# Performance work log

Hardware: AMD Instinct MI355X
Metric: run time of the kernel (lower is better)

## Reference

```python
import jax, jax.numpy as jnp
import numpy as np

B, N, F = 32, 64, 128          # batch, num_nodes, n_in_node
K, H, M, NH = 4, 256, 256, 256 # edge_types, msg_hid, msg_out, n_hid
E = N * (N - 1)                # fully-connected directed edges = 4032


def setup_inputs() -> dict:
    key = jax.random.key(0)
    ks = jax.random.split(key, 12)
    inputs = jax.random.normal(ks[0], (B, N, F), dtype=jnp.float32)
    # soft edge-type assignment per edge (rows sum to 1, as in NRI)
    rel_type = jax.nn.softmax(jax.random.normal(ks[1], (B, E, K), dtype=jnp.float32), axis=-1)
    # one-hot receiver/sender matrices for all i != j pairs
    idx = np.array([(i, j) for i in range(N) for j in range(N) if i != j], dtype=np.int64)
    eye = np.eye(N, dtype=np.float32)
    rel_rec = jnp.asarray(eye[idx[:, 0]])   # [E, N]
    rel_send = jnp.asarray(eye[idx[:, 1]])  # [E, N]
    # per-edge-type message MLP weights (stacked over K): y = x @ W + b
    W1 = jax.random.normal(ks[2], (K, 2 * F, H), dtype=jnp.float32) / np.sqrt(2 * F)
    b1 = jnp.zeros((K, H), dtype=jnp.float32)
    W2 = jax.random.normal(ks[3], (K, H, M), dtype=jnp.float32) / np.sqrt(H)
    b2 = jnp.zeros((K, M), dtype=jnp.float32)
    # output MLP
    Wo1 = jax.random.normal(ks[4], (F + M, NH), dtype=jnp.float32) / np.sqrt(F + M)
    bo1 = jnp.zeros((NH,), dtype=jnp.float32)
    Wo2 = jax.random.normal(ks[5], (NH, NH), dtype=jnp.float32) / np.sqrt(NH)
    bo2 = jnp.zeros((NH,), dtype=jnp.float32)
    Wo3 = jax.random.normal(ks[6], (NH, F), dtype=jnp.float32) / np.sqrt(NH)
    bo3 = jnp.zeros((F,), dtype=jnp.float32)
    return {"inputs": inputs, "rel_type": rel_type, "rel_rec": rel_rec, "rel_send": rel_send,
            "W1": W1, "b1": b1, "W2": W2, "b2": b2,
            "Wo1": Wo1, "bo1": bo1, "Wo2": Wo2, "bo2": bo2, "Wo3": Wo3, "bo3": bo3}


def reference(inputs, rel_type, rel_rec, rel_send, W1, b1, W2, b2, Wo1, bo1, Wo2, bo2, Wo3, bo3):
    # gather node states to edges via one-hot matmul (as in the source)
    receivers = jnp.einsum('en,bnf->bef', rel_rec, inputs)   # [B,E,F]
    senders = jnp.einsum('en,bnf->bef', rel_send, inputs)    # [B,E,F]
    pre_msg = jnp.concatenate([receivers, senders], axis=-1)  # [B,E,2F]
    # per-edge-type 2-layer ReLU MLP, batched over the K edge types
    h = jax.nn.relu(jnp.einsum('bef,kfh->bkeh', pre_msg, W1) + b1[:, None, :])  # [B,K,E,H]
    msg = jax.nn.relu(jnp.einsum('bkeh,khm->bkem', h, W2) + b2[:, None, :])     # [B,K,E,M]
    # mask by soft edge type and accumulate over types (dropout p=0 -> identity)
    all_msgs = jnp.einsum('bkem,bek->bem', msg, rel_type)     # [B,E,M]
    # scatter-aggregate messages to receiver nodes via one-hot matmul
    agg_msgs = jnp.einsum('en,bem->bnm', rel_rec, all_msgs)   # [B,N,M]
    aug = jnp.concatenate([inputs, agg_msgs], axis=-1)        # [B,N,F+M]
    p = jax.nn.relu(aug @ Wo1 + bo1)
    p = jax.nn.relu(p @ Wo2 + bo2)
    p = p @ Wo3 + bo3
    return inputs + p
```

## Files before the change

### kernel.cpp

```cpp
#include <hip/hip_runtime.h>


#define B_ 32
#define N_ 64
#define F_ 128
#define K_ 4
#define E_ 4032

#define WS_W2T 0u
#define WS_R   524288u
#define WS_S   4718592u
#define WS_AGG 8912896u

typedef unsigned short u16;
typedef u16    u16x4  __attribute__((ext_vector_type(4)));
typedef u16    u16x8  __attribute__((ext_vector_type(8)));
typedef __bf16 bf16x8 __attribute__((ext_vector_type(8)));
typedef float  f32x4  __attribute__((ext_vector_type(4)));
typedef float  f32x16 __attribute__((ext_vector_type(16)));

__device__ __forceinline__ u16 f2bf(float f) {
    unsigned u; __builtin_memcpy(&u, &f, 4);
    return (u16)((u + 0x7FFFu + ((u >> 16) & 1u)) >> 16);
}
__device__ __forceinline__ float bf2f(u16 u) {
    unsigned v = ((unsigned)u) << 16;
    float f; __builtin_memcpy(&f, &v, 4); return f;
}

#define LBAR() do { \
    asm volatile("s_waitcnt lgkmcnt(0)" ::: "memory"); \
    __builtin_amdgcn_s_barrier(); \
    __builtin_amdgcn_sched_barrier(0); \
} while (0)

__global__ __launch_bounds__(256) void prep_rs_kernel(
    const float* __restrict__ W2, const float* __restrict__ x,
    const float* __restrict__ W1, const float* __restrict__ b1,
    u16* __restrict__ W2t, u16* __restrict__ R, u16* __restrict__ S)
{
    __shared__ u16 ldsA[64 * 136];
    __shared__ u16 ldsW[32 * 136];
    const int tid = threadIdx.x;

    if (blockIdx.x < 1024) {
        unsigned gid = blockIdx.x * 256u + tid;
        unsigned chunk = gid >> 13, r = gid & 8191u;
        unsigned g = r >> 11, n = (r >> 3) & 255u, e = r & 7u;
        unsigned k = chunk >> 3, kc = chunk & 7u, ks2 = g >> 1, lhh = g & 1u;
        unsigned kk = kc * 32u + ks2 * 16u + lhh * 8u + e;
        W2t[gid] = f2bf(W2[(k * 256u + kk) * 256u + n]);
        return;
    }

    const int lane = tid & 63, w = tid >> 6;
    const int quad = lane >> 4, mloc = lane & 15;
    const int bx = blockIdx.x - 1024;
    const int k = bx >> 6, half = (bx >> 5) & 1, b = bx & 31;

    for (int idx = tid; idx < 2048; idx += 256) {
        int row = idx >> 5, c4 = idx & 31;
        f32x4 v = *(const f32x4*)&x[(b * 64 + row) * 128 + c4 * 4];
        u16x4 o;
#pragma unroll
        for (int e = 0; e < 4; ++e) o[e] = f2bf(v[e]);
        *(u16x4*)&ldsA[row * 136 + c4 * 4] = o;
    }
    __syncthreads();

    bf16x8 aF[4];
#pragma unroll
    for (int ks = 0; ks < 4; ++ks)
        aF[ks] = *(const bf16x8*)&ldsA[(w * 16 + mloc) * 136 + quad * 8 + ks * 32];

    u16* dst = half ? S : R;
    for (int c = 0; c < 8; ++c) {
        __syncthreads();
        for (int idx = tid; idx < 4096; idx += 256) {
            int n = idx & 31, f = idx >> 5;
            ldsW[n * 136 + f] = f2bf(W1[(k * 256 + half * 128 + f) * 256 + c * 32 + n]);
        }
        __syncthreads();
#pragma unroll
        for (int nt = 0; nt < 2; ++nt) {
            f32x4 acc = (f32x4){0.f, 0.f, 0.f, 0.f};
            const int boff = (nt * 16 + mloc) * 136 + quad * 8;
#pragma unroll
            for (int ks = 0; ks < 4; ++ks)
                acc = __builtin_amdgcn_mfma_f32_16x16x32_bf16(
                    aF[ks], *(const bf16x8*)&ldsW[boff + ks * 32], acc, 0, 0, 0);
            const int n = c * 32 + nt * 16 + mloc;
            const float bias = half ? 0.f : b1[k * 256 + n];
#pragma unroll
            for (int r = 0; r < 4; ++r) {
                int row = w * 16 + quad * 4 + r;
                if (half) {
                    dst[((size_t)((k * 8 + c) * 2048 + b * 64 + row)) * 32 + nt * 16 + mloc]
                        = f2bf(acc[r] + bias);
                } else {
                    dst[((size_t)(k * 2048 + b * 64 + row)) * 256 + n] = f2bf(acc[r] + bias);
                }
            }
        }
    }
}

__global__ __launch_bounds__(256, 3) void edge12_kernel(
    const u16* __restrict__ R, const u16* __restrict__ S2,
    const float* __restrict__ rel, const u16* __restrict__ W2t,
    const float* __restrict__ b2, u16* __restrict__ aggb)
{
    __shared__ u16   Hs[32][64][8];
    __shared__ float Rf[4][256];
    __shared__ float rtS[4][64];

    const int tid  = threadIdx.x;
    const int lane = tid & 63;
    const int w    = tid >> 6;
    const int l31  = lane & 31;
    const int lh   = lane >> 5;
    const int bid  = ((blockIdx.x & 7) << 8) | (blockIdx.x >> 3);
    const int b    = bid >> 6;
    const int i    = bid & 63;

    {
        const int k = tid >> 6, j = tid & 63;
        float v = 0.f;
        if (j != i) v = rel[((size_t)(b * E_) + i * 63 + (j - (j > i))) * 4 + k];
        rtS[k][j] = v;
    }
    {
        const int k = tid >> 6, e4 = tid & 63;
        u16x4 t4 = *(const u16x4*)&R[((size_t)(k * 2048 + b * 64 + i)) * 256 + e4 * 4];
#pragma unroll
        for (int e = 0; e < 4; ++e) Rf[k][e4 * 4 + e] = bf2f(t4[e]);
    }

    u16x8 sreg[8];
#pragma unroll
    for (int s = 0; s < 8; ++s)
        sreg[s] = *(const u16x8*)&S2[((size_t)(s * 2048 + b * 64 + lane)) * 32 + w * 8];

    __syncthreads();

    const u16* Wb = W2t + lh * 2048 + (w * 64 + l31) * 8;

    float amsg[2] = {0.f, 0.f};

    for (int kT = 0; kT < 4; ++kT) {
        bf16x8 Bb[2][2][2];
#pragma unroll
        for (int ks2 = 0; ks2 < 2; ++ks2) {
            const u16* wp = Wb + (size_t)(kT * 8) * 8192 + ks2 * 4096;
            Bb[0][ks2][0] = *(const bf16x8*)(wp);
            Bb[0][ks2][1] = *(const bf16x8*)(wp + 256);
        }
#pragma unroll
        for (int s = 0; s < 8; ++s) {
            const float* rp = &Rf[kT][s * 32 + w * 8];
            f32x4 r0 = *(const f32x4*)rp, r1 = *(const f32x4*)(rp + 4);
            bf16x8 o;
#pragma unroll
            for (int e = 0; e < 4; ++e) {
                o[e]     = (__bf16)fmaxf(r0[e] + bf2f(sreg[s][e]),     0.f);
                o[4 + e] = (__bf16)fmaxf(r1[e] + bf2f(sreg[s][4 + e]), 0.f);
            }
            *(bf16x8*)&Hs[s * 4 + w][lane][0] = o;
        }
        __syncthreads();

        f32x16 acc[2][2];
#pragma unroll
        for (int mt = 0; mt < 2; ++mt)
#pragma unroll
            for (int nt = 0; nt < 2; ++nt) acc[mt][nt] = (f32x16)(0.f);

#pragma unroll
        for (int kc = 0; kc < 8; ++kc) {
            const int cur = kc & 1, nxt = cur ^ 1;
            if (kc == 0 && kT < 3) {
#pragma unroll
                for (int s = 0; s < 8; ++s)
                    sreg[s] = *(const u16x8*)&S2[((size_t)(((kT + 1) * 8 + s) * 2048 + b * 64 + lane)) * 32 + w * 8];
            }
            if (kc < 7) {
#pragma unroll
                for (int ks2 = 0; ks2 < 2; ++ks2) {
                    const u16* wp = Wb + (size_t)(kT * 8 + kc + 1) * 8192 + ks2 * 4096;
                    Bb[nxt][ks2][0] = *(const bf16x8*)(wp);
                    Bb[nxt][ks2][1] = *(const bf16x8*)(wp + 256);
                }
            }
#pragma unroll
            for (int ks2 = 0; ks2 < 2; ++ks2) {
                const int g = kc * 4 + ks2 * 2 + lh;
                bf16x8 A0 = *(const bf16x8*)&Hs[g][l31][0];
                bf16x8 A1 = *(const bf16x8*)&Hs[g][32 + l31][0];
                acc[0][0] = __builtin_amdgcn_mfma_f32_32x32x16_bf16(A0, Bb[cur][ks2][0], acc[0][0], 0, 0, 0);
                acc[0][1] = __builtin_amdgcn_mfma_f32_32x32x16_bf16(A0, Bb[cur][ks2][1], acc[0][1], 0, 0, 0);
                acc[1][0] = __builtin_amdgcn_mfma_f32_32x32x16_bf16(A1, Bb[cur][ks2][0], acc[1][0], 0, 0, 0);
                acc[1][1] = __builtin_amdgcn_mfma_f32_32x32x16_bf16(A1, Bb[cur][ks2][1], acc[1][1], 0, 0, 0);
            }
        }

#pragma unroll
        for (int nt = 0; nt < 2; ++nt) {
            const float bias = b2[kT * 256 + w * 64 + nt * 32 + l31];
#pragma unroll
            for (int mt = 0; mt < 2; ++mt) {
                float s = 0.f;
#pragma unroll
                for (int rq = 0; rq < 4; ++rq) {
                    f32x4 rt4 = *(const f32x4*)&rtS[kT][mt * 32 + rq * 8 + 4 * lh];
#pragma unroll
                    for (int e = 0; e < 4; ++e) {
                        float v = acc[mt][nt][rq * 4 + e] + bias;
                        v = v > 0.f ? v : 0.f;
                        s += rt4[e] * v;
                    }
                }
                amsg[nt] += s;
            }
        }
        __syncthreads();
    }

#pragma unroll
    for (int nt = 0; nt < 2; ++nt) {
        float s = amsg[nt] + __shfl_xor(amsg[nt], 32);
        if (lh == 0)
            aggb[(size_t)(b * 64 + i) * 256 + w * 64 + nt * 32 + l31] = f2bf(s);
    }
}

__global__ __launch_bounds__(512) void outmlp4_kernel(
    const float* __restrict__ x, const u16* __restrict__ aggb,
    const float* __restrict__ Wo1, const float* __restrict__ bo1,
    const float* __restrict__ Wo2, const float* __restrict__ bo2,
    const float* __restrict__ Wo3, const float* __restrict__ bo3,
    float* __restrict__ out)
{
    __shared__ u16 wch[4][256][8];
    __shared__ u16 p1S[32 * 264];
    __shared__ u16 p2S[32 * 264];
    const int tid  = threadIdx.x, lane = tid & 63;
    const int w8   = tid >> 6;
    const int mh   = w8 >> 2;
    const int w4   = w8 & 3;
    const int quad = lane >> 4, mloc = lane & 15;
    const int row0 = blockIdx.x * 32;
    const int sg2  = (tid >> 8) * 2;
    const int sn   = tid & 255;

    {
        f32x4 acc[4];
#pragma unroll
        for (int nt = 0; nt < 4; ++nt) acc[nt] = (f32x4){0.f, 0.f, 0.f, 0.f};
        float wr[16];
#pragma unroll
        for (int g2 = 0; g2 < 2; ++g2)
#pragma unroll
            for (int e = 0; e < 8; ++e) wr[g2 * 8 + e] = Wo1[((sg2 + g2) * 8 + e) * 256 + sn];
        for (int kk = 0; kk < 12; ++kk) {
            bf16x8 aF;
            {
                const int row = row0 + mh * 16 + mloc;
                if (kk < 4) {
                    u16x8 t;
#pragma unroll
                    for (int e = 0; e < 8; ++e) t[e] = f2bf(x[row * 128 + kk * 32 + quad * 8 + e]);
                    __builtin_memcpy(&aF, &t, 16);
                } else {
                    aF = *(const bf16x8*)&aggb[(size_t)row * 256 + (kk - 4) * 32 + quad * 8];
                }
            }
#pragma unroll
            for (int g2 = 0; g2 < 2; ++g2) {
                u16x8 o;
#pragma unroll
                for (int e = 0; e < 8; ++e) o[e] = f2bf(wr[g2 * 8 + e]);
                *(u16x8*)&wch[sg2 + g2][sn][0] = o;
            }
            if (kk + 1 < 12) {
#pragma unroll
                for (int g2 = 0; g2 < 2; ++g2)
#pragma unroll
                    for (int e = 0; e < 8; ++e)
                        wr[g2 * 8 + e] = Wo1[((kk + 1) * 32 + (sg2 + g2) * 8 + e) * 256 + sn];
            }
            LBAR();
#pragma unroll
            for (int nt = 0; nt < 4; ++nt) {
                bf16x8 bF = *(const bf16x8*)&wch[quad][w4 * 64 + nt * 16 + mloc][0];
                acc[nt] = __builtin_amdgcn_mfma_f32_16x16x32_bf16(aF, bF, acc[nt], 0, 0, 0);
            }
            LBAR();
        }
#pragma unroll
        for (int nt = 0; nt < 4; ++nt) {
            const int n = w4 * 64 + nt * 16 + mloc;
            const float bias = bo1[n];
#pragma unroll
            for (int r = 0; r < 4; ++r) {
                float v = acc[nt][r] + bias;
                p1S[(mh * 16 + quad * 4 + r) * 264 + n] = f2bf(v > 0.f ? v : 0.f);
            }
        }
    }
    LBAR();
    {
        f32x4 acc[4];
#pragma unroll
        for (int nt = 0; nt < 4; ++nt) acc[nt] = (f32x4){0.f, 0.f, 0.f, 0.f};
        float wr[16];
#pragma unroll
        for (int g2 = 0; g2 < 2; ++g2)
#pragma unroll
            for (int e = 0; e < 8; ++e) wr[g2 * 8 + e] = Wo2[((sg2 + g2) * 8 + e) * 256 + sn];
        for (int kk = 0; kk < 8; ++kk) {
            bf16x8 aF = *(const bf16x8*)&p1S[(mh * 16 + mloc) * 264 + kk * 32 + quad * 8];
#pragma unroll
            for (int g2 = 0; g2 < 2; ++g2) {
                u16x8 o;
#pragma unroll
                for (int e = 0; e < 8; ++e) o[e] = f2bf(wr[g2 * 8 + e]);
                *(u16x8*)&wch[sg2 + g2][sn][0] = o;
            }
            if (kk + 1 < 8) {
#pragma unroll
                for (int g2 = 0; g2 < 2; ++g2)
#pragma unroll
                    for (int e = 0; e < 8; ++e)
                        wr[g2 * 8 + e] = Wo2[((kk + 1) * 32 + (sg2 + g2) * 8 + e) * 256 + sn];
            }
            LBAR();
#pragma unroll
            for (int nt = 0; nt < 4; ++nt) {
                bf16x8 bF = *(const bf16x8*)&wch[quad][w4 * 64 + nt * 16 + mloc][0];
                acc[nt] = __builtin_amdgcn_mfma_f32_16x16x32_bf16(aF, bF, acc[nt], 0, 0, 0);
            }
            LBAR();
        }
#pragma unroll
        for (int nt = 0; nt < 4; ++nt) {
            const int n = w4 * 64 + nt * 16 + mloc;
            const float bias = bo2[n];
#pragma unroll
            for (int r = 0; r < 4; ++r) {
                float v = acc[nt][r] + bias;
                p2S[(mh * 16 + quad * 4 + r) * 264 + n] = f2bf(v > 0.f ? v : 0.f);
            }
        }
    }
    LBAR();
    {
        f32x4 acc[2];
#pragma unroll
        for (int nt = 0; nt < 2; ++nt) acc[nt] = (f32x4){0.f, 0.f, 0.f, 0.f};
        const int sg3 = tid >> 7;
        const int sn3 = tid & 127;
        float wr[8];
#pragma unroll
        for (int e = 0; e < 8; ++e) wr[e] = Wo3[(sg3 * 8 + e) * 128 + sn3];
        for (int kk = 0; kk < 8; ++kk) {
            bf16x8 aF = *(const bf16x8*)&p2S[(mh * 16 + mloc) * 264 + kk * 32 + quad * 8];
            {
                u16x8 o;
#pragma unroll
                for (int e = 0; e < 8; ++e) o[e] = f2bf(wr[e]);
                *(u16x8*)&wch[sg3][sn3][0] = o;
            }
            if (kk + 1 < 8) {
#pragma unroll
                for (int e = 0; e < 8; ++e)
                    wr[e] = Wo3[((kk + 1) * 32 + sg3 * 8 + e) * 128 + sn3];
            }
            LBAR();
#pragma unroll
            for (int nt = 0; nt < 2; ++nt) {
                bf16x8 bF = *(const bf16x8*)&wch[quad][w4 * 32 + nt * 16 + mloc][0];
                acc[nt] = __builtin_amdgcn_mfma_f32_16x16x32_bf16(aF, bF, acc[nt], 0, 0, 0);
            }
            LBAR();
        }
#pragma unroll
        for (int nt = 0; nt < 2; ++nt) {
            const int n = w4 * 32 + nt * 16 + mloc;
            const float bias = bo3[n];
#pragma unroll
            for (int r = 0; r < 4; ++r) {
                const int grow = row0 + mh * 16 + quad * 4 + r;
                out[grow * 128 + n] = x[grow * 128 + n] + acc[nt][r] + bias;
            }
        }
    }
}

extern "C" void kernel_launch(void* const* d_in, const int* in_sizes, int n_in,
                              void* d_out, int out_size, void* d_ws, size_t ws_size,
                              hipStream_t stream) {
    const float* x   = (const float*)d_in[0];
    const float* rel = (const float*)d_in[1];
    const float* W1  = (const float*)d_in[4];
    const float* b1  = (const float*)d_in[5];
    const float* W2  = (const float*)d_in[6];
    const float* b2  = (const float*)d_in[7];
    const float* Wo1 = (const float*)d_in[8];
    const float* bo1 = (const float*)d_in[9];
    const float* Wo2 = (const float*)d_in[10];
    const float* bo2 = (const float*)d_in[11];
    const float* Wo3 = (const float*)d_in[12];
    const float* bo3 = (const float*)d_in[13];
    float* out = (float*)d_out;

    char* ws = (char*)d_ws;
    u16* W2t  = (u16*)(ws + WS_W2T);
    u16* R    = (u16*)(ws + WS_R);
    u16* S2   = (u16*)(ws + WS_S);
    u16* aggb = (u16*)(ws + WS_AGG);

    prep_rs_kernel<<<1280, 256, 0, stream>>>(W2, x, W1, b1, W2t, R, S2);
    edge12_kernel<<<2048, 256, 0, stream>>>(R, S2, rel, W2t, b2, aggb);
    outmlp4_kernel<<<64, 512, 0, stream>>>(x, aggb, Wo1, bo1, Wo2, bo2, Wo3, bo3, out);
}
```

Baseline: 196.1 us.

## Split prep work across more blocks and drop LDS staging in output MLP

The W2 transpose now reads W2 in coalesced order and scatters the writes. The R/S projection blocks are split in two along the output-column chunks, doubling the grid. The output MLP goes from 64 blocks of 32 rows with LDS-staged weights to 128 blocks of 16 rows, each wave loading its bf16 weight fragments straight from global memory with no per-step barriers. This adds parallelism and removes synchronisation, at the cost of redundant, uncoalesced global weight reads per wave and each block converting W1 columns for only half the range.

```diff
diff --git a/kernel.cpp b/kernel.cpp
--- a/kernel.cpp
+++ b/kernel.cpp
@@ -45,18 +45,20 @@
 
     if (blockIdx.x < 1024) {
         unsigned gid = blockIdx.x * 256u + tid;
-        unsigned chunk = gid >> 13, r = gid & 8191u;
-        unsigned g = r >> 11, n = (r >> 3) & 255u, e = r & 7u;
-        unsigned k = chunk >> 3, kc = chunk & 7u, ks2 = g >> 1, lhh = g & 1u;
-        unsigned kk = kc * 32u + ks2 * 16u + lhh * 8u + e;
-        W2t[gid] = f2bf(W2[(k * 256u + kk) * 256u + n]);
+        unsigned n = gid & 255u, kk = (gid >> 8) & 255u, k = gid >> 16;
+        unsigned dst = (k * 8u + (kk >> 5)) * 8192u
+                     + ((((kk >> 4) & 1u) * 2u) + ((kk >> 3) & 1u)) * 2048u
+                     + n * 8u + (kk & 7u);
+        W2t[dst] = f2bf(W2[gid]);
         return;
     }
 
     const int lane = tid & 63, w = tid >> 6;
     const int quad = lane >> 4, mloc = lane & 15;
     const int bx = blockIdx.x - 1024;
-    const int k = bx >> 6, half = (bx >> 5) & 1, b = bx & 31;
+    const int ch = bx & 1;
+    const int bq = bx >> 1;
+    const int k = bq >> 6, half = (bq >> 5) & 1, b = bq & 31;
 
     for (int idx = tid; idx < 2048; idx += 256) {
         int row = idx >> 5, c4 = idx & 31;
@@ -74,7 +76,7 @@
         aF[ks] = *(const bf16x8*)&ldsA[(w * 16 + mloc) * 136 + quad * 8 + ks * 32];
 
     u16* dst = half ? S : R;
-    for (int c = 0; c < 8; ++c) {
+    for (int c = ch * 4; c < ch * 4 + 4; ++c) {
         __syncthreads();
         for (int idx = tid; idx < 4096; idx += 256) {
             int n = idx & 31, f = idx >> 5;
@@ -233,77 +235,54 @@
     }
 }
 
-__global__ __launch_bounds__(512) void outmlp4_kernel(
+__global__ __launch_bounds__(256) void outmlp5_kernel(
     const float* __restrict__ x, const u16* __restrict__ aggb,
     const float* __restrict__ Wo1, const float* __restrict__ bo1,
     const float* __restrict__ Wo2, const float* __restrict__ bo2,
     const float* __restrict__ Wo3, const float* __restrict__ bo3,
     float* __restrict__ out)
 {
-    __shared__ u16 wch[4][256][8];
-    __shared__ u16 p1S[32 * 264];
-    __shared__ u16 p2S[32 * 264];
-    const int tid  = threadIdx.x, lane = tid & 63;
-    const int w8   = tid >> 6;
-    const int mh   = w8 >> 2;
-    const int w4   = w8 & 3;
+    __shared__ u16 p1S[16 * 264];
+    __shared__ u16 p2S[16 * 264];
+    const int tid = threadIdx.x, lane = tid & 63, w = tid >> 6;
     const int quad = lane >> 4, mloc = lane & 15;
-    const int row0 = blockIdx.x * 32;
-    const int sg2  = (tid >> 8) * 2;
-    const int sn   = tid & 255;
+    const int row0 = blockIdx.x * 16;
 
     {
         f32x4 acc[4];
 #pragma unroll
         for (int nt = 0; nt < 4; ++nt) acc[nt] = (f32x4){0.f, 0.f, 0.f, 0.f};
-        float wr[16];
-#pragma unroll
-        for (int g2 = 0; g2 < 2; ++g2)
-#pragma unroll
-            for (int e = 0; e < 8; ++e) wr[g2 * 8 + e] = Wo1[((sg2 + g2) * 8 + e) * 256 + sn];
         for (int kk = 0; kk < 12; ++kk) {
             bf16x8 aF;
-            {
-                const int row = row0 + mh * 16 + mloc;
-                if (kk < 4) {
-                    u16x8 t;
-#pragma unroll
-                    for (int e = 0; e < 8; ++e) t[e] = f2bf(x[row * 128 + kk * 32 + quad * 8 + e]);
-                    __builtin_memcpy(&aF, &t, 16);
-                } else {
-                    aF = *(const bf16x8*)&aggb[(size_t)row * 256 + (kk - 4) * 32 + quad * 8];
-                }
-            }
-#pragma unroll
-            for (int g2 = 0; g2 < 2; ++g2) {
-                u16x8 o;
-#pragma unroll
-                for (int e = 0; e < 8; ++e) o[e] = f2bf(wr[g2 * 8 + e]);
-                *(u16x8*)&wch[sg2 + g2][sn][0] = o;
-            }
-            if (kk + 1 < 12) {
-#pragma unroll
-                for (int g2 = 0; g2 < 2; ++g2)
-#pragma unroll
-                    for (int e = 0; e < 8; ++e)
-                        wr[g2 * 8 + e] = Wo1[((kk + 1) * 32 + (sg2 + g2) * 8 + e) * 256 + sn];
-            }
-            LBAR();
+            const int row = row0 + mloc;
+            if (kk < 4) {
+                u16x8 t;
+#pragma unroll
+                for (int e = 0; e < 8; ++e) t[e] = f2bf(x[row * 128 + kk * 32 + quad * 8 + e]);
+                __builtin_memcpy(&aF, &t, 16);
+            } else {
+                aF = *(const bf16x8*)&aggb[(size_t)row * 256 + (kk - 4) * 32 + quad * 8];
+            }
 #pragma unroll
             for (int nt = 0; nt < 4; ++nt) {
-                bf16x8 bF = *(const bf16x8*)&wch[quad][w4 * 64 + nt * 16 + mloc][0];
+                const int n = w * 64 + nt * 16 + mloc;
+                u16x8 t;
+#pragma unroll
+                for (int e = 0; e < 8; ++e)
+                    t[e] = f2bf(Wo1[(kk * 32 + quad * 8 + e) * 256 + n]);
+                bf16x8 bF;
+                __builtin_memcpy(&bF, &t, 16);
                 acc[nt] = __builtin_amdgcn_mfma_f32_16x16x32_bf16(aF, bF, acc[nt], 0, 0, 0);
             }
-            LBAR();
         }
 #pragma unroll
         for (int nt = 0; nt < 4; ++nt) {
-            const int n = w4 * 64 + nt * 16 + mloc;
+            const int n = w * 64 + nt * 16 + mloc;
             const float bias = bo1[n];
 #pragma unroll
             for (int r = 0; r < 4; ++r) {
                 float v = acc[nt][r] + bias;
-                p1S[(mh * 16 + quad * 4 + r) * 264 + n] = f2bf(v > 0.f ? v : 0.f);
+                p1S[(quad * 4 + r) * 264 + n] = f2bf(v > 0.f ? v : 0.f);
             }
         }
     }
@@ -312,43 +291,28 @@
         f32x4 acc[4];
 #pragma unroll
         for (int nt = 0; nt < 4; ++nt) acc[nt] = (f32x4){0.f, 0.f, 0.f, 0.f};
-        float wr[16];
-#pragma unroll
-        for (int g2 = 0; g2 < 2; ++g2)
-#pragma unroll
-            for (int e = 0; e < 8; ++e) wr[g2 * 8 + e] = Wo2[((sg2 + g2) * 8 + e) * 256 + sn];
         for (int kk = 0; kk < 8; ++kk) {
-            bf16x8 aF = *(const bf16x8*)&p1S[(mh * 16 + mloc) * 264 + kk * 32 + quad * 8];
-#pragma unroll
-            for (int g2 = 0; g2 < 2; ++g2) {
-                u16x8 o;
-#pragma unroll
-                for (int e = 0; e < 8; ++e) o[e] = f2bf(wr[g2 * 8 + e]);
-                *(u16x8*)&wch[sg2 + g2][sn][0] = o;
-            }
-            if (kk + 1 < 8) {
-#pragma unroll
-                for (int g2 = 0; g2 < 2; ++g2)
-#pragma unroll
-                    for (int e = 0; e < 8; ++e)
-                        wr[g2 * 8 + e] = Wo2[((kk + 1) * 32 + (sg2 + g2) * 8 + e) * 256 + sn];
-            }
-            LBAR();
+            bf16x8 aF = *(const bf16x8*)&p1S[mloc * 264 + kk * 32 + quad * 8];
 #pragma unroll
             for (int nt = 0; nt < 4; ++nt) {
-                bf16x8 bF = *(const bf16x8*)&wch[quad][w4 * 64 + nt * 16 + mloc][0];
+                const int n = w * 64 + nt * 16 + mloc;
+                u16x8 t;
+#pragma unroll
+                for (int e = 0; e < 8; ++e)
+                    t[e] = f2bf(Wo2[(kk * 32 + quad * 8 + e) * 256 + n]);
+                bf16x8 bF;
+                __builtin_memcpy(&bF, &t, 16);
                 acc[nt] = __builtin_amdgcn_mfma_f32_16x16x32_bf16(aF, bF, acc[nt], 0, 0, 0);
             }
-            LBAR();
         }
 #pragma unroll
         for (int nt = 0; nt < 4; ++nt) {
-            const int n = w4 * 64 + nt * 16 + mloc;
+            const int n = w * 64 + nt * 16 + mloc;
             const float bias = bo2[n];
 #pragma unroll
             for (int r = 0; r < 4; ++r) {
                 float v = acc[nt][r] + bias;
-                p2S[(mh * 16 + quad * 4 + r) * 264 + n] = f2bf(v > 0.f ? v : 0.f);
+                p2S[(quad * 4 + r) * 264 + n] = f2bf(v > 0.f ? v : 0.f);
             }
         }
     }
@@ -357,39 +321,27 @@
         f32x4 acc[2];
 #pragma unroll
         for (int nt = 0; nt < 2; ++nt) acc[nt] = (f32x4){0.f, 0.f, 0.f, 0.f};
-        const int sg3 = tid >> 7;
-        const int sn3 = tid & 127;
-        float wr[8];
-#pragma unroll
-        for (int e = 0; e < 8; ++e) wr[e] = Wo3[(sg3 * 8 + e) * 128 + sn3];
         for (int kk = 0; kk < 8; ++kk) {
-            bf16x8 aF = *(const bf16x8*)&p2S[(mh * 16 + mloc) * 264 + kk * 32 + quad * 8];
-            {
-                u16x8 o;
-#pragma unroll
-                for (int e = 0; e < 8; ++e) o[e] = f2bf(wr[e]);
-                *(u16x8*)&wch[sg3][sn3][0] = o;
-            }
-            if (kk + 1 < 8) {
+            bf16x8 aF = *(const bf16x8*)&p2S[mloc * 264 + kk * 32 + quad * 8];
+#pragma unroll
+            for (int nt = 0; nt < 2; ++nt) {
+                const int n = w * 32 + nt * 16 + mloc;
+                u16x8 t;
 #pragma unroll
                 for (int e = 0; e < 8; ++e)
-                    wr[e] = Wo3[((kk + 1) * 32 + sg3 * 8 + e) * 128 + sn3];
-            }
-            LBAR();
-#pragma unroll
-            for (int nt = 0; nt < 2; ++nt) {
-                bf16x8 bF = *(const bf16x8*)&wch[quad][w4 * 32 + nt * 16 + mloc][0];
+                    t[e] = f2bf(Wo3[(kk * 32 + quad * 8 + e) * 128 + n]);
+                bf16x8 bF;
+                __builtin_memcpy(&bF, &t, 16);
                 acc[nt] = __builtin_amdgcn_mfma_f32_16x16x32_bf16(aF, bF, acc[nt], 0, 0, 0);
             }
-            LBAR();
         }
 #pragma unroll
         for (int nt = 0; nt < 2; ++nt) {
-            const int n = w4 * 32 + nt * 16 + mloc;
+            const int n = w * 32 + nt * 16 + mloc;
             const float bias = bo3[n];
 #pragma unroll
             for (int r = 0; r < 4; ++r) {
-                const int grow = row0 + mh * 16 + quad * 4 + r;
+                const int grow = row0 + quad * 4 + r;
                 out[grow * 128 + n] = x[grow * 128 + n] + acc[nt][r] + bias;
             }
         }
@@ -419,7 +371,7 @@
     u16* S2   = (u16*)(ws + WS_S);
     u16* aggb = (u16*)(ws + WS_AGG);
 
-    prep_rs_kernel<<<1280, 256, 0, stream>>>(W2, x, W1, b1, W2t, R, S2);
+    prep_rs_kernel<<<1536, 256, 0, stream>>>(W2, x, W1, b1, W2t, R, S2);
     edge12_kernel<<<2048, 256, 0, stream>>>(R, S2, rel, W2t, b2, aggb);
-    outmlp4_kernel<<<64, 512, 0, stream>>>(x, aggb, Wo1, bo1, Wo2, bo2, Wo3, bo3, out);
-}
+    outmlp5_kernel<<<128, 256, 0, stream>>>(x, aggb, Wo1, bo1, Wo2, bo2, Wo3, bo3, out);
+}
```

Result: no change. 193.3 us (-1.4%).
